# Performance work log

Measured on AMD Instinct MI355X. Metric: run time of the kernel, lower is better.

Reference implementation:

```python
import jax, jax.numpy as jnp
import numpy as np

V = 300000        # nr lattice vertices
C = 64            # val_dim == nr_filters
FE = 9            # filter_extent = 2*(pos_dim+1)+1 for pos_dim=3, neighbourhood_size=1
GROUPS = 32
EPS = 1e-5


def setup_inputs() -> dict:
    key = jax.random.key(0)
    k1, k2, k3, k4 = jax.random.split(key, 4)
    lv = jax.random.normal(k1, (V, C), dtype=jnp.float32)
    # neighbour index table: column 0 is the center vertex itself, rest are random lattice neighbours
    rnd = jax.random.randint(k2, (V, FE), 0, V, dtype=jnp.int32)
    neigh = rnd.at[:, 0].set(jnp.arange(V, dtype=jnp.int32))
    gamma = jnp.ones((C,), dtype=jnp.float32)
    beta = jnp.zeros((C,), dtype=jnp.float32)
    weight = jax.random.normal(k3, (FE, C), dtype=jnp.float32) * (1.0 / np.sqrt(FE))
    bias = jax.random.normal(k4, (C,), dtype=jnp.float32) * 0.1
    return {"lv": lv, "neigh": neigh, "gamma": gamma, "beta": beta,
            "weight": weight, "bias": bias}


def reference(lv, neigh, gamma, beta, weight, bias):
    v, c = lv.shape
    # GroupNorm over [1, C, V]: stats per group over (channels_in_group, all vertices)
    x = lv.reshape(v, GROUPS, c // GROUPS)
    mean = jnp.mean(x, axis=(0, 2), keepdims=True)
    var = jnp.mean(jnp.square(x - mean), axis=(0, 2), keepdims=True)
    xn = (x - mean) * jax.lax.rsqrt(var + EPS)
    lv_n = xn.reshape(v, c) * gamma + beta
    # ReLU
    lv_r = jnp.maximum(lv_n, 0.0)
    # depthwise lattice conv: gather FE neighbours per vertex, per-channel weights
    gathered = lv_r[neigh]                       # [V, FE, C]
    out = jnp.einsum('vfc,fc->vc', gathered, weight) + bias
    return out
```

## Files before the change

### kernel.cpp

```cpp
#include <hip/hip_runtime.h>

#define V_N     300000
#define C_N     64
#define FE_N    9
#define NGROUPS 32
#define EPS_F   1e-5f
#define NB1     1024


__global__ __launch_bounds__(256) void k_partial(const float4* __restrict__ lv4,
                                                 float* __restrict__ psum) {
    const int tid  = threadIdx.x;
    const int c4   = tid & 15;
    const int vrow = tid >> 4;

    float4 s = make_float4(0.f, 0.f, 0.f, 0.f);
    float4 q = make_float4(0.f, 0.f, 0.f, 0.f);
    for (int v = blockIdx.x * 16 + vrow; v < V_N; v += gridDim.x * 16) {
        float4 x = lv4[v * 16 + c4];
        s.x += x.x; s.y += x.y; s.z += x.z; s.w += x.w;
        q.x += x.x * x.x; q.y += x.y * x.y; q.z += x.z * x.z; q.w += x.w * x.w;
    }

    __shared__ float lds[256 * 8];
    float* p = &lds[tid * 8];
    p[0] = s.x; p[1] = s.y; p[2] = s.z; p[3] = s.w;
    p[4] = q.x; p[5] = q.y; p[6] = q.z; p[7] = q.w;
    __syncthreads();

    if (tid < 16) {
        float as[4] = {0.f, 0.f, 0.f, 0.f};
        float aq[4] = {0.f, 0.f, 0.f, 0.f};
        for (int i = 0; i < 16; ++i) {
            const float* r = &lds[(i * 16 + tid) * 8];
            as[0] += r[0]; as[1] += r[1]; as[2] += r[2]; as[3] += r[3];
            aq[0] += r[4]; aq[1] += r[5]; aq[2] += r[6]; aq[3] += r[7];
        }
        float* o = &psum[(size_t)blockIdx.x * 128];
        o[4 * tid + 0]      = as[0]; o[4 * tid + 1]      = as[1];
        o[4 * tid + 2]      = as[2]; o[4 * tid + 3]      = as[3];
        o[64 + 4 * tid + 0] = aq[0]; o[64 + 4 * tid + 1] = aq[1];
        o[64 + 4 * tid + 2] = aq[2]; o[64 + 4 * tid + 3] = aq[3];
    }
}

__global__ __launch_bounds__(256) void k_stats(const float* __restrict__ psum,
                                               const float* __restrict__ gamma,
                                               const float* __restrict__ beta,
                                               float* __restrict__ stats) {
    const int g  = blockIdx.x;
    const int c0 = 2 * g, c1 = 2 * g + 1;
    const int t  = threadIdx.x;

    float S = 0.f, Q = 0.f;
    for (int b = t; b < NB1; b += 256) {
        const float* r = &psum[(size_t)b * 128];
        S += r[c0] + r[c1];
        Q += r[64 + c0] + r[64 + c1];
    }
    #pragma unroll
    for (int off = 32; off > 0; off >>= 1) {
        S += __shfl_down(S, off, 64);
        Q += __shfl_down(Q, off, 64);
    }
    __shared__ float ls[8];
    const int wave = t >> 6, lane = t & 63;
    if (lane == 0) { ls[wave] = S; ls[4 + wave] = Q; }
    __syncthreads();
    if (t == 0) {
        float St = ls[0] + ls[1] + ls[2] + ls[3];
        float Qt = ls[4] + ls[5] + ls[6] + ls[7];
        const float inv = 1.0f / (2.0f * (float)V_N);
        float mean = St * inv;
        float var  = Qt * inv - mean * mean;
        float rsd  = rsqrtf(var + EPS_F);
        float sc0 = gamma[c0] * rsd, sc1 = gamma[c1] * rsd;
        stats[c0]      = sc0;
        stats[c1]      = sc1;
        stats[64 + c0] = beta[c0] - mean * sc0;
        stats[64 + c1] = beta[c1] - mean * sc1;
    }
}

__global__ __launch_bounds__(256) void k_conv(const float4* __restrict__ lv4,
                                              const int* __restrict__ neigh,
                                              const float4* __restrict__ w4,
                                              const float4* __restrict__ bias4,
                                              const float* __restrict__ stats,
                                              float4* __restrict__ out4) {
    const int tid   = threadIdx.x;
    const int c4    = tid & 15;
    const int vloc  = tid >> 4;
    const int vbase = blockIdx.x * 16;

    __shared__ int nb[16 * FE_N];
    if (tid < 16 * FE_N) nb[tid] = neigh[(size_t)vbase * FE_N + tid];

    const float4* s4p = (const float4*)stats;
    const float4 sc = s4p[c4];
    const float4 sh = s4p[16 + c4];

    float4 w[FE_N];
    #pragma unroll
    for (int f = 0; f < FE_N; ++f) w[f] = w4[f * 16 + c4];

    float4 acc = bias4[c4];
    __syncthreads();

    int u[FE_N];
    #pragma unroll
    for (int f = 0; f < FE_N; ++f) u[f] = nb[vloc * FE_N + f];

    float4 x[FE_N];
    #pragma unroll
    for (int f = 0; f < FE_N; ++f) x[f] = lv4[(size_t)u[f] * 16 + c4];

    #pragma unroll
    for (int f = 0; f < FE_N; ++f) {
        float4 r;
        r.x = fmaxf(fmaf(x[f].x, sc.x, sh.x), 0.f);
        r.y = fmaxf(fmaf(x[f].y, sc.y, sh.y), 0.f);
        r.z = fmaxf(fmaf(x[f].z, sc.z, sh.z), 0.f);
        r.w = fmaxf(fmaf(x[f].w, sc.w, sh.w), 0.f);
        acc.x = fmaf(r.x, w[f].x, acc.x);
        acc.y = fmaf(r.y, w[f].y, acc.y);
        acc.z = fmaf(r.z, w[f].z, acc.z);
        acc.w = fmaf(r.w, w[f].w, acc.w);
    }
    out4[(size_t)(vbase + vloc) * 16 + c4] = acc;
}

extern "C" void kernel_launch(void* const* d_in, const int* in_sizes, int n_in,
                              void* d_out, int out_size, void* d_ws, size_t ws_size,
                              hipStream_t stream) {
    const float* lv     = (const float*)d_in[0];
    const int*   neigh  = (const int*)d_in[1];
    const float* gamma  = (const float*)d_in[2];
    const float* beta   = (const float*)d_in[3];
    const float* weight = (const float*)d_in[4];
    const float* bias   = (const float*)d_in[5];
    float*       out    = (float*)d_out;
    float*       ws     = (float*)d_ws;

    float* psum  = ws;
    float* stats = ws + NB1 * 128;

    k_partial<<<NB1, 256, 0, stream>>>((const float4*)lv, psum);
    k_stats<<<NGROUPS, 256, 0, stream>>>(psum, gamma, beta, stats);
    k_conv<<<V_N / 16, 256, 0, stream>>>((const float4*)lv, neigh,
                                         (const float4*)weight,
                                         (const float4*)bias, stats,
                                         (float4*)out);
}
```

Baseline: 237.7 us.

## Precompute normalized ReLU activations in fp16 and gather them in conv

Adds a pass that applies GroupNorm scale/shift and ReLU once per element and writes the result as fp16 into workspace. The conv kernel then gathers 8-byte half4 values instead of 16-byte float4, which halves the bytes moved by the random 9-way gather and drops the per-neighbour norm arithmetic. The cost is one extra streaming read of the input plus a write of the fp16 copy, and reduced precision in the activations. It falls back to the old fp32 path when the workspace is too small.

```diff
diff --git a/kernel.cpp b/kernel.cpp
--- a/kernel.cpp
+++ b/kernel.cpp
@@ -7,6 +7,12 @@
 #define EPS_F   1e-5f
 #define NB1     1024
 
+typedef _Float16 half4_t __attribute__((ext_vector_type(4)));
+
+#define PSUM_F   (NB1 * 128)
+#define STATS_F  (PSUM_F)
+#define G_F      (PSUM_F + 128)
+#define WS_NEED  ((size_t)G_F * 4 + (size_t)V_N * C_N * 2)
 
 __global__ __launch_bounds__(256) void k_partial(const float4* __restrict__ lv4,
                                                  float* __restrict__ psum) {
@@ -82,12 +88,67 @@
     }
 }
 
-__global__ __launch_bounds__(256) void k_conv(const float4* __restrict__ lv4,
-                                              const int* __restrict__ neigh,
-                                              const float4* __restrict__ w4,
-                                              const float4* __restrict__ bias4,
+__global__ __launch_bounds__(256) void k_norm(const float4* __restrict__ lv4,
                                               const float* __restrict__ stats,
-                                              float4* __restrict__ out4) {
+                                              half4_t* __restrict__ g) {
+    const int i  = blockIdx.x * 256 + threadIdx.x;
+    const int c4 = i & 15;
+    const float4* s4 = (const float4*)stats;
+    const float4 sc = s4[c4];
+    const float4 sh = s4[16 + c4];
+    float4 x = lv4[i];
+    half4_t h;
+    h.x = (_Float16)fmaxf(fmaf(x.x, sc.x, sh.x), 0.f);
+    h.y = (_Float16)fmaxf(fmaf(x.y, sc.y, sh.y), 0.f);
+    h.z = (_Float16)fmaxf(fmaf(x.z, sc.z, sh.z), 0.f);
+    h.w = (_Float16)fmaxf(fmaf(x.w, sc.w, sh.w), 0.f);
+    g[i] = h;
+}
+
+__global__ __launch_bounds__(256) void k_conv_h(const half4_t* __restrict__ g,
+                                                const int* __restrict__ neigh,
+                                                const float4* __restrict__ w4,
+                                                const float4* __restrict__ bias4,
+                                                float4* __restrict__ out4) {
+    const int tid   = threadIdx.x;
+    const int c4    = tid & 15;
+    const int vloc  = tid >> 4;
+    const int vbase = blockIdx.x * 16;
+
+    __shared__ int nb[16 * FE_N];
+    if (tid < 16 * FE_N) nb[tid] = neigh[(size_t)vbase * FE_N + tid];
+
+    float4 w[FE_N];
+    #pragma unroll
+    for (int f = 0; f < FE_N; ++f) w[f] = w4[f * 16 + c4];
+
+    float4 acc = bias4[c4];
+    __syncthreads();
+
+    int u[FE_N];
+    #pragma unroll
+    for (int f = 0; f < FE_N; ++f) u[f] = nb[vloc * FE_N + f];
+
+    half4_t x[FE_N];
+    #pragma unroll
+    for (int f = 0; f < FE_N; ++f) x[f] = g[(size_t)u[f] * 16 + c4];
+
+    #pragma unroll
+    for (int f = 0; f < FE_N; ++f) {
+        acc.x = fmaf((float)x[f].x, w[f].x, acc.x);
+        acc.y = fmaf((float)x[f].y, w[f].y, acc.y);
+        acc.z = fmaf((float)x[f].z, w[f].z, acc.z);
+        acc.w = fmaf((float)x[f].w, w[f].w, acc.w);
+    }
+    out4[(size_t)(vbase + vloc) * 16 + c4] = acc;
+}
+
+__global__ __launch_bounds__(256) void k_conv_f32(const float4* __restrict__ lv4,
+                                                  const int* __restrict__ neigh,
+                                                  const float4* __restrict__ w4,
+                                                  const float4* __restrict__ bias4,
+                                                  const float* __restrict__ stats,
+                                                  float4* __restrict__ out4) {
     const int tid   = threadIdx.x;
     const int c4    = tid & 15;
     const int vloc  = tid >> 4;
@@ -142,13 +203,23 @@
     float*       out    = (float*)d_out;
     float*       ws     = (float*)d_ws;
 
-    float* psum  = ws;
-    float* stats = ws + NB1 * 128;
+    float*   psum  = ws;
+    float*   stats = ws + STATS_F;
+    half4_t* g     = (half4_t*)(ws + G_F);
 
     k_partial<<<NB1, 256, 0, stream>>>((const float4*)lv, psum);
     k_stats<<<NGROUPS, 256, 0, stream>>>(psum, gamma, beta, stats);
-    k_conv<<<V_N / 16, 256, 0, stream>>>((const float4*)lv, neigh,
-                                         (const float4*)weight,
-                                         (const float4*)bias, stats,
-                                         (float4*)out);
-}
+
+    if (ws_size >= WS_NEED) {
+        k_norm<<<(V_N * 16) / 256, 256, 0, stream>>>((const float4*)lv, stats, g);
+        k_conv_h<<<V_N / 16, 256, 0, stream>>>(g, neigh,
+                                               (const float4*)weight,
+                                               (const float4*)bias,
+                                               (float4*)out);
+    } else {
+        k_conv_f32<<<V_N / 16, 256, 0, stream>>>((const float4*)lv, neigh,
+                                                 (const float4*)weight,
+                                                 (const float4*)bias, stats,
+                                                 (float4*)out);
+    }
+}
```

After: 221.3 us. 6.9% less time.

## Cast lattice values to fp16 in stats pass and gather halves in conv

Applied to the files above, without the earlier changes.

The stats pass now also writes an fp16 copy of the input to workspace, and the conv kernel gathers 16-byte half8 chunks (8 channels per thread, 32 vertices per block) instead of float4, with weights staged in LDS. This is meant to halve the bytes moved by the random 9-way neighbour gather, which dominates traffic. The cost is an extra write of the half copy and reduced input precision before normalization. A fallback to the original fp32 path is kept for when the workspace is too small.

```diff
diff --git a/kernel.cpp b/kernel.cpp
--- a/kernel.cpp
+++ b/kernel.cpp
@@ -7,9 +7,17 @@
 #define EPS_F   1e-5f
 #define NB1     1024
 
-
-__global__ __launch_bounds__(256) void k_partial(const float4* __restrict__ lv4,
-                                                 float* __restrict__ psum) {
+typedef _Float16 half4_t __attribute__((ext_vector_type(4)));
+typedef _Float16 half8_t __attribute__((ext_vector_type(8)));
+
+#define PSUM_F   (NB1 * 128)
+#define STATS_F  (PSUM_F)
+#define G_F      (PSUM_F + 128)
+#define WS_NEED  ((size_t)G_F * 4 + (size_t)V_N * C_N * 2)
+
+__global__ __launch_bounds__(256) void k_partial_cast(const float4* __restrict__ lv4,
+                                                      float* __restrict__ psum,
+                                                      half4_t* __restrict__ h) {
     const int tid  = threadIdx.x;
     const int c4   = tid & 15;
     const int vrow = tid >> 4;
@@ -20,6 +28,10 @@
         float4 x = lv4[v * 16 + c4];
         s.x += x.x; s.y += x.y; s.z += x.z; s.w += x.w;
         q.x += x.x * x.x; q.y += x.y * x.y; q.z += x.z * x.z; q.w += x.w * x.w;
+        half4_t hv;
+        hv.x = (_Float16)x.x; hv.y = (_Float16)x.y;
+        hv.z = (_Float16)x.z; hv.w = (_Float16)x.w;
+        h[v * 16 + c4] = hv;
     }
 
     __shared__ float lds[256 * 8];
@@ -44,6 +56,42 @@
     }
 }
 
+__global__ __launch_bounds__(256) void k_partial(const float4* __restrict__ lv4,
+                                                 float* __restrict__ psum) {
+    const int tid  = threadIdx.x;
+    const int c4   = tid & 15;
+    const int vrow = tid >> 4;
+
+    float4 s = make_float4(0.f, 0.f, 0.f, 0.f);
+    float4 q = make_float4(0.f, 0.f, 0.f, 0.f);
+    for (int v = blockIdx.x * 16 + vrow; v < V_N; v += gridDim.x * 16) {
+        float4 x = lv4[v * 16 + c4];
+        s.x += x.x; s.y += x.y; s.z += x.z; s.w += x.w;
+        q.x += x.x * x.x; q.y += x.y * x.y; q.z += x.z * x.z; q.w += x.w * x.w;
+    }
+
+    __shared__ float lds[256 * 8];
+    float* p = &lds[tid * 8];
+    p[0] = s.x; p[1] = s.y; p[2] = s.z; p[3] = s.w;
+    p[4] = q.x; p[5] = q.y; p[6] = q.z; p[7] = q.w;
+    __syncthreads();
+
+    if (tid < 16) {
+        float as[4] = {0.f, 0.f, 0.f, 0.f};
+        float aq[4] = {0.f, 0.f, 0.f, 0.f};
+        for (int i = 0; i < 16; ++i) {
+            const float* r = &lds[(i * 16 + tid) * 8];
+            as[0] += r[0]; as[1] += r[1]; as[2] += r[2]; as[3] += r[3];
+            aq[0] += r[4]; aq[1] += r[5]; aq[2] += r[6]; aq[3] += r[7];
+        }
+        float* o = &psum[(size_t)blockIdx.x * 128];
+        o[4 * tid + 0]      = as[0]; o[4 * tid + 1]      = as[1];
+        o[4 * tid + 2]      = as[2]; o[4 * tid + 3]      = as[3];
+        o[64 + 4 * tid + 0] = aq[0]; o[64 + 4 * tid + 1] = aq[1];
+        o[64 + 4 * tid + 2] = aq[2]; o[64 + 4 * tid + 3] = aq[3];
+    }
+}
+
 __global__ __launch_bounds__(256) void k_stats(const float* __restrict__ psum,
                                                const float* __restrict__ gamma,
                                                const float* __restrict__ beta,
@@ -82,12 +130,72 @@
     }
 }
 
-__global__ __launch_bounds__(256) void k_conv(const float4* __restrict__ lv4,
-                                              const int* __restrict__ neigh,
-                                              const float4* __restrict__ w4,
-                                              const float4* __restrict__ bias4,
-                                              const float* __restrict__ stats,
-                                              float4* __restrict__ out4) {
+__global__ __launch_bounds__(256) void k_conv_h8(const half8_t* __restrict__ h,
+                                                 const int* __restrict__ neigh,
+                                                 const float* __restrict__ weight,
+                                                 const float4* __restrict__ bias4,
+                                                 const float* __restrict__ stats,
+                                                 float4* __restrict__ out4) {
+    const int tid   = threadIdx.x;
+    const int c8    = tid & 7;
+    const int vloc  = tid >> 3;
+    const int vbase = blockIdx.x * 32;
+
+    __shared__ int   nb[32 * FE_N];
+    __shared__ float wl[FE_N * C_N];
+    for (int i = tid; i < 32 * FE_N; i += 256) nb[i] = neigh[(size_t)vbase * FE_N + i];
+    for (int i = tid; i < FE_N * C_N; i += 256) wl[i] = weight[i];
+
+    const float4* s4 = (const float4*)stats;
+    const float4 scA = s4[c8 * 2],      scB = s4[c8 * 2 + 1];
+    const float4 shA = s4[16 + c8 * 2], shB = s4[17 + c8 * 2];
+    const float4 bA  = bias4[c8 * 2],   bB  = bias4[c8 * 2 + 1];
+
+    __syncthreads();
+
+    int u[FE_N];
+    #pragma unroll
+    for (int f = 0; f < FE_N; ++f) u[f] = nb[vloc * FE_N + f];
+
+    half8_t x[FE_N];
+    #pragma unroll
+    for (int f = 0; f < FE_N; ++f) x[f] = h[(size_t)u[f] * 8 + c8];
+
+    float4 accA = bA, accB = bB;
+    const float4* wl4 = (const float4*)wl;
+    #pragma unroll
+    for (int f = 0; f < FE_N; ++f) {
+        float4 wA = wl4[f * 16 + c8 * 2];
+        float4 wB = wl4[f * 16 + c8 * 2 + 1];
+        float4 rA, rB;
+        rA.x = fmaxf(fmaf((float)x[f].s0, scA.x, shA.x), 0.f);
+        rA.y = fmaxf(fmaf((float)x[f].s1, scA.y, shA.y), 0.f);
+        rA.z = fmaxf(fmaf((float)x[f].s2, scA.z, shA.z), 0.f);
+        rA.w = fmaxf(fmaf((float)x[f].s3, scA.w, shA.w), 0.f);
+        rB.x = fmaxf(fmaf((float)x[f].s4, scB.x, shB.x), 0.f);
+        rB.y = fmaxf(fmaf((float)x[f].s5, scB.y, shB.y), 0.f);
+        rB.z = fmaxf(fmaf((float)x[f].s6, scB.z, shB.z), 0.f);
+        rB.w = fmaxf(fmaf((float)x[f].s7, scB.w, shB.w), 0.f);
+        accA.x = fmaf(rA.x, wA.x, accA.x);
+        accA.y = fmaf(rA.y, wA.y, accA.y);
+        accA.z = fmaf(rA.z, wA.z, accA.z);
+        accA.w = fmaf(rA.w, wA.w, accA.w);
+        accB.x = fmaf(rB.x, wB.x, accB.x);
+        accB.y = fmaf(rB.y, wB.y, accB.y);
+        accB.z = fmaf(rB.z, wB.z, accB.z);
+        accB.w = fmaf(rB.w, wB.w, accB.w);
+    }
+    const size_t ob = (size_t)(vbase + vloc) * 16 + c8 * 2;
+    out4[ob]     = accA;
+    out4[ob + 1] = accB;
+}
+
+__global__ __launch_bounds__(256) void k_conv_f32(const float4* __restrict__ lv4,
+                                                  const int* __restrict__ neigh,
+                                                  const float4* __restrict__ w4,
+                                                  const float4* __restrict__ bias4,
+                                                  const float* __restrict__ stats,
+                                                  float4* __restrict__ out4) {
     const int tid   = threadIdx.x;
     const int c4    = tid & 15;
     const int vloc  = tid >> 4;
@@ -142,13 +250,22 @@
     float*       out    = (float*)d_out;
     float*       ws     = (float*)d_ws;
 
-    float* psum  = ws;
-    float* stats = ws + NB1 * 128;
-
-    k_partial<<<NB1, 256, 0, stream>>>((const float4*)lv, psum);
-    k_stats<<<NGROUPS, 256, 0, stream>>>(psum, gamma, beta, stats);
-    k_conv<<<V_N / 16, 256, 0, stream>>>((const float4*)lv, neigh,
-                                         (const float4*)weight,
-                                         (const float4*)bias, stats,
-                                         (float4*)out);
-}
+    float*   psum  = ws;
+    float*   stats = ws + STATS_F;
+    half4_t* h     = (half4_t*)(ws + G_F);
+
+    if (ws_size >= WS_NEED) {
+        k_partial_cast<<<NB1, 256, 0, stream>>>((const float4*)lv, psum, h);
+        k_stats<<<NGROUPS, 256, 0, stream>>>(psum, gamma, beta, stats);
+        k_conv_h8<<<V_N / 32, 256, 0, stream>>>((const half8_t*)h, neigh, weight,
+                                                (const float4*)bias, stats,
+                                                (float4*)out);
+    } else {
+        k_partial<<<NB1, 256, 0, stream>>>((const float4*)lv, psum);
+        k_stats<<<NGROUPS, 256, 0, stream>>>(psum, gamma, beta, stats);
+        k_conv_f32<<<V_N / 16, 256, 0, stream>>>((const float4*)lv, neigh,
+                                                 (const float4*)weight,
+                                                 (const float4*)bias, stats,
+                                                 (float4*)out);
+    }
+}
```

Result: faster. 201.8 us (-15.1%).
